# Kernel optimization log

Hardware: AMD Instinct MI355X
Metric: run time of the kernel (lower is better)

The kernel has to match this reference:

```python
import jax, jax.numpy as jnp
import numpy as np

N = 50000
E = 1600000
IN_F = 512
OUT_F = 128
NEG_SLOPE = 0.01   # nn.LeakyReLU() default
TEMPERATURE = 0.5


def setup_inputs() -> dict:
    key = jax.random.key(0)
    k1, k2, k3, k4 = jax.random.split(key, 4)
    h = jax.random.normal(k1, (N, IN_F), dtype=jnp.float32)
    # xavier_uniform with gain=1.414
    limW = 1.414 * np.sqrt(6.0 / (IN_F + OUT_F))
    W = jax.random.uniform(k2, (IN_F, OUT_F), minval=-limW, maxval=limW, dtype=jnp.float32)
    lima = 1.414 * np.sqrt(6.0 / (2 * OUT_F + 1))
    a = jax.random.uniform(k3, (2 * OUT_F, 1), minval=-lima, maxval=lima, dtype=jnp.float32)
    edge_index = jax.random.randint(k4, (2, E), 0, N, dtype=jnp.int64)
    return {"h": h, "W": W, "a": a, "edge_index": edge_index}


def reference(h, W, a, edge_index):
    # Inference: F.dropout(training=False) is identity.
    Wh = h @ W                                   # [N, F_out]
    src = edge_index[0]                          # row indices -> softmax segments
    dst = edge_index[1]
    # cat([Wh[src], Wh[dst]]) @ a == (Wh @ a1)[src] + (Wh @ a2)[dst]
    a1 = a[:OUT_F, 0]
    a2 = a[OUT_F:, 0]
    s1 = Wh @ a1                                 # [N]
    s2 = Wh @ a2                                 # [N]
    e = s1[src] + s2[dst]                        # [E]
    e = jnp.where(e >= 0, e, NEG_SLOPE * e)      # LeakyReLU
    logits = e / TEMPERATURE
    # sparse softmax over dim=1 (per source-node row segments)
    seg_max = jax.ops.segment_max(logits, src, num_segments=N)  # [N]
    ex = jnp.exp(logits - seg_max[src])          # [E]
    denom = jax.ops.segment_sum(ex, src, num_segments=N)        # [N]
    att = ex / denom[src]                        # [E]
    # sparse-dense matmul: h_prime[i] = sum_j att(i,j) * Wh[j]
    h_prime = jax.ops.segment_sum(att[:, None] * Wh[dst], src, num_segments=N)  # [N, F_out]
    return jax.nn.relu(h_prime)                  # concat=True path
```

## Files before the change

### kernel.cpp

```cpp
#include <hip/hip_runtime.h>
#include <cstdint>
#include <cstddef>

#define N_NODES 50000
#define N_EDGES 1600000
#define IN_FEAT 512
#define OUT_FEAT 128
#define NEG_SLOPE 0.01f
#define INV_TEMP 2.0f
#define PAD_DEG 128

#define BUCKETS 400
#define BNODES 125
#define BCAP 5000
#define A_BLOCKS 500
#define A_EPC (N_EDGES / A_BLOCKS)
#define A_G4 (A_EPC / 4)

#define CONV_BLOCKS ((IN_FEAT * OUT_FEAT) / 256)
#define GEMM_BLOCKS ((N_NODES + 127) / 128)

typedef __attribute__((ext_vector_type(8))) short short8;
typedef __attribute__((ext_vector_type(4))) float f32x4;

#define GLOBAL_AS __attribute__((address_space(1)))
#define LDS_AS __attribute__((address_space(3)))

__device__ inline unsigned short f2bf(float x) {
    unsigned int u = __float_as_uint(x);
    unsigned int r = (u + 0x7fffu + ((u >> 16) & 1u)) >> 16;
    return (unsigned short)r;
}
__device__ inline float bf2f(unsigned short b) {
    return __uint_as_float(((unsigned int)b) << 16);
}


__global__ __launch_bounds__(256) void build_kernel(const float* __restrict__ W,
                                                    unsigned short* __restrict__ Wt,
                                                    const int* __restrict__ src,
                                                    const int* __restrict__ dst,
                                                    int* __restrict__ bucket_cursor,
                                                    int* __restrict__ binned) {
    __shared__ int cntL[BUCKETS];
    __shared__ int baseL[BUCKETS];

    if (blockIdx.x >= A_BLOCKS) {
        int tid = (blockIdx.x - A_BLOCKS) * 256 + threadIdx.x;
        if (tid < IN_FEAT * OUT_FEAT) {
            int n = tid >> 9;
            int k = tid & 511;
            Wt[tid] = f2bf(W[k * OUT_FEAT + n]);
        }
        return;
    }

    int t = threadIdx.x;
    for (int i = t; i < BUCKETS; i += 256) cntL[i] = 0;
    __syncthreads();
    size_t ebase = (size_t)blockIdx.x * A_EPC;

    for (int g = t; g < A_G4; g += 256) {
        int4 s4 = *(const int4*)(src + ebase + (size_t)g * 4);
#pragma unroll
        for (int j = 0; j < 4; ++j) {
            int s = (&s4.x)[j];
            atomicAdd(&cntL[s / BNODES], 1);
        }
    }
    __syncthreads();
    for (int i = t; i < BUCKETS; i += 256) {
        int c = cntL[i];
        baseL[i] = c ? atomicAdd(&bucket_cursor[i], c) : 0;
        cntL[i] = 0;
    }
    __syncthreads();
    for (int g = t; g < A_G4; g += 256) {
        int4 s4 = *(const int4*)(src + ebase + (size_t)g * 4);
        int4 d4 = *(const int4*)(dst + ebase + (size_t)g * 4);
#pragma unroll
        for (int j = 0; j < 4; ++j) {
            int s = (&s4.x)[j];
            int b = s / BNODES;
            int sl = s - b * BNODES;
            int pos = atomicAdd(&cntL[b], 1);
            int slot = baseL[b] + pos;
            if (slot < BCAP)
                binned[(size_t)b * BCAP + slot] = (sl << 16) | (&d4.x)[j];
        }
    }
}


__global__ __launch_bounds__(512) void gemm_binB_kernel(const float* __restrict__ h,
                                                        const unsigned short* __restrict__ Wt,
                                                        const float* __restrict__ a_vec,
                                                        unsigned short* __restrict__ Whb,
                                                        float* __restrict__ s1,
                                                        float* __restrict__ s2,
                                                        const int* __restrict__ bucket_cursor,
                                                        const int* __restrict__ binned,
                                                        int* __restrict__ cnt,
                                                        int* __restrict__ csr) {
    __shared__ unsigned short lB[3][8 * 2 * 64 * 8];

    if (blockIdx.x < BUCKETS) {
        int* cL = (int*)&lB[0][0];
        int b = blockIdx.x;
        int t = threadIdx.x;
        if (t < BNODES) cL[t] = 0;
        __syncthreads();
        int m = min(bucket_cursor[b], BCAP);
        const int* bp = binned + (size_t)b * BCAP;
        int n0 = b * BNODES;
        for (int i = t; i < m; i += 512) {
            int p = bp[i];
            int sl = p >> 16;
            int d = p & 0xFFFF;
            int pos = atomicAdd(&cL[sl], 1);
            if (pos < PAD_DEG) csr[(size_t)(n0 + sl) * PAD_DEG + pos] = d;
        }
        __syncthreads();
        if (t < BNODES) cnt[n0 + t] = min(cL[t], PAD_DEG);
        return;
    }

    int bid = blockIdx.x - BUCKETS;
    int t = threadIdx.x;
    int w = t >> 6;
    int L = t & 63;
    int m0 = bid * 128;

    int arow = m0 + w * 16 + (L & 15);
    int arow_c = arow < N_NODES ? arow : N_NODES - 1;
    int kq = (L >> 4) * 8;
    const float* arp = h + (size_t)arow_c * IN_FEAT + kq;

    f32x4 acc[8];
#pragma unroll
    for (int i = 0; i < 8; ++i) acc[i] = (f32x4){0.f, 0.f, 0.f, 0.f};

    auto stageB = [&](int slot, int k0) {
#pragma unroll
        for (int ksub = 0; ksub < 2; ++ksub) {
            const GLOBAL_AS unsigned short* g =
                (const GLOBAL_AS unsigned short*)(Wt + (size_t)(w * 16 + (L & 15)) * IN_FEAT +
                                                  (k0 + ksub * 32 + kq));
            LDS_AS unsigned short* lp = (LDS_AS unsigned short*)(&lB[slot][(w * 2 + ksub) * 512]);
            __builtin_amdgcn_global_load_lds((const GLOBAL_AS void*)g, (LDS_AS void*)lp, 16, 0, 0);
        }
    };
    auto loadA = [&](int step, float4 out[4]) {
        const float* p = arp + step * 64;
        out[0] = *(const float4*)(p);
        out[1] = *(const float4*)(p + 4);
        out[2] = *(const float4*)(p + 32);
        out[3] = *(const float4*)(p + 36);
    };
    auto convA = [&](const float4 a[4], short8& f0, short8& f1) {
        short8 v;
        v[0] = (short)f2bf(a[0].x); v[1] = (short)f2bf(a[0].y);
        v[2] = (short)f2bf(a[0].z); v[3] = (short)f2bf(a[0].w);
        v[4] = (short)f2bf(a[1].x); v[5] = (short)f2bf(a[1].y);
        v[6] = (short)f2bf(a[1].z); v[7] = (short)f2bf(a[1].w);
        f0 = v;
        v[0] = (short)f2bf(a[2].x); v[1] = (short)f2bf(a[2].y);
        v[2] = (short)f2bf(a[2].z); v[3] = (short)f2bf(a[2].w);
        v[4] = (short)f2bf(a[3].x); v[5] = (short)f2bf(a[3].y);
        v[6] = (short)f2bf(a[3].z); v[7] = (short)f2bf(a[3].w);
        f1 = v;
    };

    float4 avA[4], avB[4], avC[4];
#pragma unroll
    for (int q = 0; q < 4; ++q) avC[q] = make_float4(0.f, 0.f, 0.f, 0.f);

    stageB(0, 0);
    asm volatile("" ::: "memory");
    stageB(1, 64);
    loadA(0, avA);
    loadA(1, avB);
    asm volatile("s_waitcnt vmcnt(10)" ::: "memory");
    __builtin_amdgcn_s_barrier();

#pragma unroll
    for (int it = 0; it < 8; ++it) {
        if (it < 6) {
            stageB((it + 2) % 3, (it + 2) * 64);
            loadA(it + 2, avC);
        }

        short8 af0, af1;
        convA(avA, af0, af1);

        const int buf = it % 3;
#pragma unroll
        for (int nb = 0; nb < 8; ++nb) {
            short8 bf = *(const short8*)(&lB[buf][((nb * 2 + 0) * 64 + L) * 8]);
            acc[nb] = __builtin_amdgcn_mfma_f32_16x16x32_bf16(af0, bf, acc[nb], 0, 0, 0);
        }
#pragma unroll
        for (int nb = 0; nb < 8; ++nb) {
            short8 bf = *(const short8*)(&lB[buf][((nb * 2 + 1) * 64 + L) * 8]);
            acc[nb] = __builtin_amdgcn_mfma_f32_16x16x32_bf16(af1, bf, acc[nb], 0, 0, 0);
        }

#pragma unroll
        for (int q = 0; q < 4; ++q) { avA[q] = avB[q]; avB[q] = avC[q]; }

        if (it < 6) {
            asm volatile("s_waitcnt vmcnt(6)" ::: "memory");
            __builtin_amdgcn_s_barrier();
        } else if (it == 6) {
            asm volatile("s_waitcnt vmcnt(0)" ::: "memory");
            __builtin_amdgcn_s_barrier();
        }
    }

    int col0 = L & 15;
    int rbase = m0 + w * 16 + (L >> 4) * 4;

    float a1c[8], a2c[8];
#pragma unroll
    for (int nb = 0; nb < 8; ++nb) {
        a1c[nb] = a_vec[nb * 16 + col0];
        a2c[nb] = a_vec[128 + nb * 16 + col0];
    }

#pragma unroll
    for (int r = 0; r < 4; ++r) {
        int row = rbase + r;
        bool ok = row < N_NODES;
        float p1 = 0.f, p2 = 0.f;
        if (ok) {
            unsigned short* orow = Whb + (size_t)row * OUT_FEAT;
#pragma unroll
            for (int nb = 0; nb < 8; ++nb) {
                float v = acc[nb][r];
                orow[nb * 16 + col0] = f2bf(v);
                p1 = fmaf(v, a1c[nb], p1);
                p2 = fmaf(v, a2c[nb], p2);
            }
        }
#pragma unroll
        for (int off = 8; off > 0; off >>= 1) {
            p1 += __shfl_xor(p1, off, 64);
            p2 += __shfl_xor(p2, off, 64);
        }
        if (ok && col0 == 0) {
            s1[row] = p1;
            s2[row] = p2;
        }
    }
}


__global__ __launch_bounds__(256) void node_kernel(const unsigned short* __restrict__ Whb,
                                                   const float* __restrict__ s1,
                                                   const float* __restrict__ s2,
                                                   const int* __restrict__ cnt,
                                                   const int* __restrict__ csr,
                                                   float* __restrict__ out) {
    int lane = threadIdx.x & 63;
    int w = threadIdx.x >> 6;
    int n = blockIdx.x * 4 + w;
    if (n >= N_NODES) return;
    int deg = cnt[n];
    size_t start = (size_t)n * PAD_DEG;
    int g = lane >> 4;
    int fo = lane & 15;

    float accv[8];
#pragma unroll
    for (int f = 0; f < 8; ++f) accv[f] = 0.f;
    float inv = 0.f;

    if (deg > 0) {
        float s1n = s1[n];
        int d0 = 0, d1 = 0;
        float ex0 = 0.f, ex1 = 0.f;
        if (lane < deg) {
            d0 = csr[start + lane];
            float ev = s1n + s2[d0];
            ev = ev >= 0.f ? ev : NEG_SLOPE * ev;
            ex0 = __expf(ev * INV_TEMP);
        }
        if (lane + 64 < deg) {
            d1 = csr[start + lane + 64];
            float ev = s1n + s2[d1];
            ev = ev >= 0.f ? ev : NEG_SLOPE * ev;
            ex1 = __expf(ev * INV_TEMP);
        }
        float denom = ex0 + ex1;
#pragma unroll
        for (int off = 32; off > 0; off >>= 1) denom += __shfl_xor(denom, off, 64);
        inv = 1.0f / denom;

#pragma unroll 2
        for (int jj = 0; jj < deg; jj += 8) {
            int e0 = jj + g;
            int e1 = jj + 4 + g;
            bool hi0 = jj >= 64;
            bool hi1 = (jj + 4) >= 64;
            float p0 = __shfl(hi0 ? ex1 : ex0, e0 & 63, 64);
            int dd0 = __shfl(hi0 ? d1 : d0, e0 & 63, 64);
            float p1 = __shfl(hi1 ? ex1 : ex0, e1 & 63, 64);
            int dd1 = __shfl(hi1 ? d1 : d0, e1 & 63, 64);
            short8 row0 = *(const short8*)(Whb + (size_t)dd0 * OUT_FEAT + fo * 8);
            short8 row1 = *(const short8*)(Whb + (size_t)dd1 * OUT_FEAT + fo * 8);
#pragma unroll
            for (int f = 0; f < 8; ++f)
                accv[f] = fmaf(p0, bf2f((unsigned short)row0[f]), accv[f]);
#pragma unroll
            for (int f = 0; f < 8; ++f)
                accv[f] = fmaf(p1, bf2f((unsigned short)row1[f]), accv[f]);
        }
#pragma unroll
        for (int f = 0; f < 8; ++f) {
            accv[f] += __shfl_xor(accv[f], 16, 64);
            accv[f] += __shfl_xor(accv[f], 32, 64);
        }
    }

    if (g == 0) {
        float* orow = out + (size_t)n * OUT_FEAT + fo * 8;
        float4 o0, o1;
        o0.x = fmaxf(accv[0] * inv, 0.f); o0.y = fmaxf(accv[1] * inv, 0.f);
        o0.z = fmaxf(accv[2] * inv, 0.f); o0.w = fmaxf(accv[3] * inv, 0.f);
        o1.x = fmaxf(accv[4] * inv, 0.f); o1.y = fmaxf(accv[5] * inv, 0.f);
        o1.z = fmaxf(accv[6] * inv, 0.f); o1.w = fmaxf(accv[7] * inv, 0.f);
        *(float4*)(orow) = o0;
        *(float4*)(orow + 4) = o1;
    }
}


extern "C" void kernel_launch(void* const* d_in, const int* in_sizes, int n_in,
                              void* d_out, int out_size, void* d_ws, size_t ws_size,
                              hipStream_t stream) {
    const float* h = (const float*)d_in[0];
    const float* W = (const float*)d_in[1];
    const float* a = (const float*)d_in[2];
    const int* edge = (const int*)d_in[3];
    const int* src = edge;
    const int* dst = edge + N_EDGES;
    float* out = (float*)d_out;

    char* ws = (char*)d_ws;
    size_t off = 0;
    auto alloc = [&](size_t bytes) -> void* {
        void* p = ws + off;
        off = (off + bytes + 255) & ~(size_t)255;
        return p;
    };
    unsigned short* Whb = (unsigned short*)alloc((size_t)N_NODES * OUT_FEAT * sizeof(unsigned short));
    float* s1 = (float*)alloc((size_t)N_NODES * sizeof(float));
    float* s2 = (float*)alloc((size_t)N_NODES * sizeof(float));
    int* cnt = (int*)alloc((size_t)N_NODES * sizeof(int));
    int* csr = (int*)alloc((size_t)N_NODES * PAD_DEG * sizeof(int));
    unsigned short* Wt = (unsigned short*)alloc((size_t)IN_FEAT * OUT_FEAT * sizeof(unsigned short));
    int* bucket_cursor = (int*)alloc((size_t)BUCKETS * sizeof(int));
    int* binned = (int*)alloc((size_t)BUCKETS * BCAP * sizeof(int));

    hipMemsetAsync(bucket_cursor, 0, BUCKETS * sizeof(int), stream);
    build_kernel<<<A_BLOCKS + CONV_BLOCKS, 256, 0, stream>>>(W, Wt, src, dst, bucket_cursor, binned);
    gemm_binB_kernel<<<BUCKETS + GEMM_BLOCKS, 512, 0, stream>>>(h, Wt, a, Whb, s1, s2,
                                                                bucket_cursor, binned, cnt, csr);
    node_kernel<<<(N_NODES + 3) / 4, 256, 0, stream>>>(Whb, s1, s2, cnt, csr, out);
}
```

Before: 259.1 us.

## Co-schedule edge binning pass A with GEMM and split bin pass B out

Moves the edge bucketing pass (count plus scatter into buckets) out of the weight-conversion kernel and into the GEMM launch as extra blocks. The bandwidth-bound binning then overlaps with the compute-bound GEMM. The per-bucket CSR build becomes a separate small kernel, and the memset of the bucket cursors is folded into the weight-conversion kernel. This adds one kernel launch, and the binning blocks, which use 512 threads, now compete with GEMM blocks for CU resources.

```diff
diff --git a/kernel.cpp b/kernel.cpp
--- a/kernel.cpp
+++ b/kernel.cpp
@@ -36,96 +36,72 @@
 }
 
 
-__global__ __launch_bounds__(256) void build_kernel(const float* __restrict__ W,
+__global__ __launch_bounds__(256) void convw_kernel(const float* __restrict__ W,
                                                     unsigned short* __restrict__ Wt,
-                                                    const int* __restrict__ src,
-                                                    const int* __restrict__ dst,
-                                                    int* __restrict__ bucket_cursor,
-                                                    int* __restrict__ binned) {
-    __shared__ int cntL[BUCKETS];
-    __shared__ int baseL[BUCKETS];
-
-    if (blockIdx.x >= A_BLOCKS) {
-        int tid = (blockIdx.x - A_BLOCKS) * 256 + threadIdx.x;
-        if (tid < IN_FEAT * OUT_FEAT) {
-            int n = tid >> 9;
-            int k = tid & 511;
-            Wt[tid] = f2bf(W[k * OUT_FEAT + n]);
-        }
-        return;
-    }
-
-    int t = threadIdx.x;
-    for (int i = t; i < BUCKETS; i += 256) cntL[i] = 0;
-    __syncthreads();
-    size_t ebase = (size_t)blockIdx.x * A_EPC;
-
-    for (int g = t; g < A_G4; g += 256) {
-        int4 s4 = *(const int4*)(src + ebase + (size_t)g * 4);
-#pragma unroll
-        for (int j = 0; j < 4; ++j) {
-            int s = (&s4.x)[j];
-            atomicAdd(&cntL[s / BNODES], 1);
-        }
-    }
-    __syncthreads();
-    for (int i = t; i < BUCKETS; i += 256) {
-        int c = cntL[i];
-        baseL[i] = c ? atomicAdd(&bucket_cursor[i], c) : 0;
-        cntL[i] = 0;
-    }
-    __syncthreads();
-    for (int g = t; g < A_G4; g += 256) {
-        int4 s4 = *(const int4*)(src + ebase + (size_t)g * 4);
-        int4 d4 = *(const int4*)(dst + ebase + (size_t)g * 4);
-#pragma unroll
-        for (int j = 0; j < 4; ++j) {
-            int s = (&s4.x)[j];
-            int b = s / BNODES;
-            int sl = s - b * BNODES;
-            int pos = atomicAdd(&cntL[b], 1);
-            int slot = baseL[b] + pos;
-            if (slot < BCAP)
-                binned[(size_t)b * BCAP + slot] = (sl << 16) | (&d4.x)[j];
-        }
-    }
-}
-
-
-__global__ __launch_bounds__(512) void gemm_binB_kernel(const float* __restrict__ h,
+                                                    int* __restrict__ bucket_cursor) {
+    int tid = blockIdx.x * 256 + threadIdx.x;
+    if (tid < BUCKETS) bucket_cursor[tid] = 0;
+    if (tid < IN_FEAT * OUT_FEAT) {
+        int n = tid >> 9;
+        int k = tid & 511;
+        Wt[tid] = f2bf(W[k * OUT_FEAT + n]);
+    }
+}
+
+
+__global__ __launch_bounds__(512) void gemm_binA_kernel(const float* __restrict__ h,
                                                         const unsigned short* __restrict__ Wt,
                                                         const float* __restrict__ a_vec,
                                                         unsigned short* __restrict__ Whb,
                                                         float* __restrict__ s1,
                                                         float* __restrict__ s2,
-                                                        const int* __restrict__ bucket_cursor,
-                                                        const int* __restrict__ binned,
-                                                        int* __restrict__ cnt,
-                                                        int* __restrict__ csr) {
+                                                        const int* __restrict__ src,
+                                                        const int* __restrict__ dst,
+                                                        int* __restrict__ bucket_cursor,
+                                                        int* __restrict__ binned) {
     __shared__ unsigned short lB[3][8 * 2 * 64 * 8];
 
-    if (blockIdx.x < BUCKETS) {
-        int* cL = (int*)&lB[0][0];
-        int b = blockIdx.x;
+    if (blockIdx.x >= GEMM_BLOCKS) {
+        int* cntL = (int*)&lB[0][0];
+        int* baseL = cntL + BUCKETS;
         int t = threadIdx.x;
-        if (t < BNODES) cL[t] = 0;
+        for (int i = t; i < BUCKETS; i += 512) cntL[i] = 0;
         __syncthreads();
-        int m = min(bucket_cursor[b], BCAP);
-        const int* bp = binned + (size_t)b * BCAP;
-        int n0 = b * BNODES;
-        for (int i = t; i < m; i += 512) {
-            int p = bp[i];
-            int sl = p >> 16;
-            int d = p & 0xFFFF;
-            int pos = atomicAdd(&cL[sl], 1);
-            if (pos < PAD_DEG) csr[(size_t)(n0 + sl) * PAD_DEG + pos] = d;
+        size_t ebase = (size_t)(blockIdx.x - GEMM_BLOCKS) * A_EPC;
+
+        for (int g = t; g < A_G4; g += 512) {
+            int4 s4 = *(const int4*)(src + ebase + (size_t)g * 4);
+#pragma unroll
+            for (int j = 0; j < 4; ++j) {
+                int s = (&s4.x)[j];
+                atomicAdd(&cntL[s / BNODES], 1);
+            }
         }
         __syncthreads();
-        if (t < BNODES) cnt[n0 + t] = min(cL[t], PAD_DEG);
+        for (int i = t; i < BUCKETS; i += 512) {
+            int c = cntL[i];
+            baseL[i] = c ? atomicAdd(&bucket_cursor[i], c) : 0;
+            cntL[i] = 0;
+        }
+        __syncthreads();
+        for (int g = t; g < A_G4; g += 512) {
+            int4 s4 = *(const int4*)(src + ebase + (size_t)g * 4);
+            int4 d4 = *(const int4*)(dst + ebase + (size_t)g * 4);
+#pragma unroll
+            for (int j = 0; j < 4; ++j) {
+                int s = (&s4.x)[j];
+                int b = s / BNODES;
+                int sl = s - b * BNODES;
+                int pos = atomicAdd(&cntL[b], 1);
+                int slot = baseL[b] + pos;
+                if (slot < BCAP)
+                    binned[(size_t)b * BCAP + slot] = (sl << 16) | (&d4.x)[j];
+            }
+        }
         return;
     }
 
-    int bid = blockIdx.x - BUCKETS;
+    int bid = blockIdx.x;
     int t = threadIdx.x;
     int w = t >> 6;
     int L = t & 63;
@@ -255,6 +231,30 @@
 }
 
 
+__global__ __launch_bounds__(256) void binB_kernel(const int* __restrict__ bucket_cursor,
+                                                   const int* __restrict__ binned,
+                                                   int* __restrict__ cnt,
+                                                   int* __restrict__ csr) {
+    __shared__ int cL[BNODES];
+    int b = blockIdx.x;
+    int t = threadIdx.x;
+    if (t < BNODES) cL[t] = 0;
+    __syncthreads();
+    int m = min(bucket_cursor[b], BCAP);
+    const int* bp = binned + (size_t)b * BCAP;
+    int n0 = b * BNODES;
+    for (int i = t; i < m; i += 256) {
+        int p = bp[i];
+        int sl = p >> 16;
+        int d = p & 0xFFFF;
+        int pos = atomicAdd(&cL[sl], 1);
+        if (pos < PAD_DEG) csr[(size_t)(n0 + sl) * PAD_DEG + pos] = d;
+    }
+    __syncthreads();
+    if (t < BNODES) cnt[n0 + t] = min(cL[t], PAD_DEG);
+}
+
+
 __global__ __launch_bounds__(256) void node_kernel(const unsigned short* __restrict__ Whb,
                                                    const float* __restrict__ s1,
                                                    const float* __restrict__ s2,
@@ -362,9 +362,9 @@
     int* bucket_cursor = (int*)alloc((size_t)BUCKETS * sizeof(int));
     int* binned = (int*)alloc((size_t)BUCKETS * BCAP * sizeof(int));
 
-    hipMemsetAsync(bucket_cursor, 0, BUCKETS * sizeof(int), stream);
-    build_kernel<<<A_BLOCKS + CONV_BLOCKS, 256, 0, stream>>>(W, Wt, src, dst, bucket_cursor, binned);
-    gemm_binB_kernel<<<BUCKETS + GEMM_BLOCKS, 512, 0, stream>>>(h, Wt, a, Whb, s1, s2,
-                                                                bucket_cursor, binned, cnt, csr);
+    convw_kernel<<<CONV_BLOCKS, 256, 0, stream>>>(W, Wt, bucket_cursor);
+    gemm_binA_kernel<<<GEMM_BLOCKS + A_BLOCKS, 512, 0, stream>>>(h, Wt, a, Whb, s1, s2,
+                                                                 src, dst, bucket_cursor, binned);
+    binB_kernel<<<BUCKETS, 256, 0, stream>>>(bucket_cursor, binned, cnt, csr);
     node_kernel<<<(N_NODES + 3) / 4, 256, 0, stream>>>(Whb, s1, s2, cnt, csr, out);
 }
```

Measured after the change: 244.6 us. 5.6% less time.
